# Performance work log

Measured on AMD Instinct MI355X. Metric: run time of the kernel, lower is better.

The kernel has to match this reference:

```python
import jax, jax.numpy as jnp
import numpy as np

NUM_CLASSES = 3
EPS = 1e-6
POS_IOU = 0.5   # assumed thresholds of utils.match_anchors_to_targets
NEG_IOU = 0.4
NEG_RATIO = 3


def _make_anchors(H, W, stride):
    sizes = np.array([3.0, 4.0, 5.0]) * stride  # 3 anchors per location
    ys = (np.arange(H) + 0.5) * stride
    xs = (np.arange(W) + 0.5) * stride
    cy, cx = np.meshgrid(ys, xs, indexing='ij')
    cx = cx[:, :, None]
    cy = cy[:, :, None]
    s = sizes[None, None, :]
    boxes = np.stack([cx - s / 2, cy - s / 2, cx + s / 2, cy + s / 2], axis=-1)  # [H,W,A,4]
    return boxes.reshape(-1, 4).astype(np.float32)


def setup_inputs() -> dict:
    key = jax.random.key(0)
    B, G, A, C = 64, 32, 3, NUM_CLASSES
    scales = [(128, 128, 8), (64, 64, 16), (32, 32, 32)]
    ks = jax.random.split(key, 6)
    inp = {}
    for i, (H, W, s) in enumerate(scales):
        inp[f'pred{i}'] = jax.random.normal(ks[i], (B, A * (5 + C), H, W), jnp.float32)
        inp[f'anchors{i}'] = jnp.asarray(_make_anchors(H, W, s))
    c = jax.random.uniform(ks[3], (B, G, 2), minval=100.0, maxval=900.0)
    wh = jax.random.uniform(ks[4], (B, G, 2), minval=16.0, maxval=200.0)
    inp['gt_boxes'] = jnp.concatenate([c - wh / 2, c + wh / 2], axis=-1)
    inp['gt_labels'] = jax.random.randint(ks[5], (B, G), 0, C)
    return inp


def _smooth_l1(x):
    ax = jnp.abs(x)
    return jnp.where(ax < 1.0, 0.5 * x * x, ax - 0.5)


def _bce_logits(x, t):
    return jnp.maximum(x, 0.0) - x * t + jnp.log1p(jnp.exp(-jnp.abs(x)))


def _pairwise_iou(a, b):  # a [N,4], b [G,4] -> [N,G]
    lt = jnp.maximum(a[:, None, :2], b[None, :, :2])
    rb = jnp.minimum(a[:, None, 2:], b[None, :, 2:])
    wh = jnp.clip(rb - lt, 0.0)
    inter = wh[..., 0] * wh[..., 1]
    area_a = (a[:, 2] - a[:, 0]) * (a[:, 3] - a[:, 1])
    area_b = (b[:, 2] - b[:, 0]) * (b[:, 3] - b[:, 1])
    return inter / (area_a[:, None] + area_b[None, :] - inter + 1e-9)


def _per_image(p, anc, gtb, gtl):
    # p: [N, 5+C], anc: [N,4], gtb: [G,4], gtl: [G]
    iou = _pairwise_iou(anc, gtb)
    best_iou = jnp.max(iou, axis=1)
    best_idx = jnp.argmax(iou, axis=1)
    m_boxes = gtb[best_idx]
    m_labels = gtl[best_idx]
    pos = best_iou >= POS_IOU
    neg = best_iou < NEG_IOU
    posf = pos.astype(p.dtype)

    ax = (anc[:, 0] + anc[:, 2]) * 0.5
    ay = (anc[:, 1] + anc[:, 3]) * 0.5
    aw = jnp.maximum(anc[:, 2] - anc[:, 0], EPS)
    ah = jnp.maximum(anc[:, 3] - anc[:, 1], EPS)
    gx = (m_boxes[:, 0] + m_boxes[:, 2]) * 0.5
    gy = (m_boxes[:, 1] + m_boxes[:, 3]) * 0.5
    gw = jnp.maximum(m_boxes[:, 2] - m_boxes[:, 0], EPS)
    gh = jnp.maximum(m_boxes[:, 3] - m_boxes[:, 1], EPS)
    t_tx = (gx - ax) / aw
    t_ty = (gy - ay) / ah
    t_tw = jnp.log(gw / aw)
    t_th = jnp.log(gh / ah)

    loc = (posf * (_smooth_l1(p[:, 0] - t_tx) + _smooth_l1(p[:, 1] - t_ty)
                   + _smooth_l1(p[:, 2] - t_tw) + _smooth_l1(p[:, 3] - t_th))).sum()

    obj_all = _bce_logits(p[:, 4], posf)
    # hard negative mining on detached loss: top (3*max(1,num_pos)) negatives
    num_pos = pos.sum()
    num_keep = NEG_RATIO * jnp.maximum(1, num_pos)
    neg_loss = jnp.where(neg, jax.lax.stop_gradient(obj_all), -1e9)
    order = jnp.argsort(-neg_loss)
    N = order.shape[0]
    ranks = jnp.zeros((N,), dtype=jnp.int32).at[order].set(jnp.arange(N, dtype=jnp.int32))
    selected = neg & (ranks < num_keep)
    obj = (obj_all * (posf + selected.astype(p.dtype))).sum()

    logp = jax.nn.log_softmax(p[:, 5:], axis=-1)
    tgt = jnp.maximum(m_labels, 0)
    ce = -jnp.take_along_axis(logp, tgt[:, None], axis=1)[:, 0]
    cls = (posf * ce).sum()
    return loc, obj, cls


def reference(pred0, pred1, pred2, anchors0, anchors1, anchors2, gt_boxes, gt_labels):
    B = pred0.shape[0]
    C = NUM_CLASSES
    total = jnp.float32(0.0)
    for pred, anc in ((pred0, anchors0), (pred1, anchors1), (pred2, anchors2)):
        N = anc.shape[0]
        p = pred.transpose(0, 2, 3, 1).reshape(B, N, 5 + C)  # [B, H*W*A, 5+C]
        loc, obj, cls = jax.vmap(lambda pb, gb, gl, a=anc: _per_image(pb, a, gb, gl))(
            p, gt_boxes, gt_labels)
        total = total + loc.sum() + obj.sum() + cls.sum()
    return total / jnp.maximum(1.0, float(B))
```

## Files before the change

kernel.cpp:

```cpp
#include <hip/hip_runtime.h>
#include <math.h>

#define BLK 256
#define SBLK 1024
#define NBINS 2048
#define CSH 42
#define QMASK ((1ULL << CSH) - 1ULL)

__device__ __forceinline__ float bce_logits(float x, float t){
    return fmaxf(x, 0.f) - x * t + log1pf(expf(-fabsf(x)));
}
__device__ __forceinline__ float smooth_l1(float x){
    float ax = fabsf(x);
    return ax < 1.f ? 0.5f * x * x : ax - 0.5f;
}

__global__ __launch_bounds__(BLK)
void det_map_all(const float* __restrict__ pred0,
                 const float* __restrict__ pred1,
                 const float* __restrict__ pred2,
                 const float* __restrict__ gtb,
                 const int*   __restrict__ gtl,
                 float* __restrict__ vals,
                 int*   __restrict__ pos_cnt,
                 double* __restrict__ accum,
                 int B)
{
    const int b  = blockIdx.y;
    const int bx = blockIdx.x;

    const float* pred; int s, qloc, P, logW; float stride_f; size_t vbase;
    if (bx < 48){      s=0; pred=pred0; P=16384; logW=7; stride_f= 8.f; qloc= bx      << 8; vbase=(size_t)b*49152; }
    else if (bx < 60){ s=1; pred=pred1; P= 4096; logW=6; stride_f=16.f; qloc=(bx-48) << 8; vbase=(size_t)B*49152 + (size_t)b*12288; }
    else {             s=2; pred=pred2; P= 1024; logW=5; stride_f=32.f; qloc=(bx-60) << 8; vbase=(size_t)B*49152 + (size_t)B*12288 + (size_t)b*3072; }

    const int tid = threadIdx.x;
    const int lq  = 2*logW - 2;
    const int Q4  = 1 << lq;
    const int a   = qloc >> lq;
    const int q   = qloc - a*Q4 + tid;
    const int pix0 = q << 2;

    const float half = 0.5f * (float)(3 + a) * stride_f;

    const int pixLo = (qloc - a*Q4) << 2;
    const int y0 = pixLo >> logW, y1 = (pixLo + BLK*4 - 1) >> logW;
    const float ymin = ((float)y0 + 0.5f) * stride_f - half;
    const float ymax = ((float)y1 + 0.5f) * stride_f + half;

    __shared__ float4 sg[32];
    __shared__ float  sarea[32];
    __shared__ int    sl[32];
    __shared__ int    s_cnt;

    {
        bool keep = false; float4 G;
        if (tid < 32){
            G = ((const float4*)gtb)[b * 32 + tid];
            keep = (G.y < ymax) && (G.w > ymin);
        }
        unsigned long long m = __ballot(keep);
        if (tid < 64){
            if (keep){
                int idx = (int)__popcll(m & ((1ULL << tid) - 1ULL));
                sg[idx] = G;
                sarea[idx] = (G.z - G.x) * (G.w - G.y);
                sl[idx] = gtl[b * 32 + tid];
            }
            if (tid == 0) s_cnt = (int)__popcll(m);
        }
    }
    __syncthreads();
    const int cnt = s_cnt;

    const int x0 = pix0 & ((1 << logW) - 1);
    const int y  = pix0 >> logW;
    const float cy = ((float)y + 0.5f) * stride_f;
    const float Ay = cy - half, Aw2 = cy + half;
    const float sz = 2.f * half;
    const float area_a = sz * sz;

    float ax[4], az[4];
    #pragma unroll
    for (int j = 0; j < 4; ++j){
        float cx = ((float)(x0 + j) + 0.5f) * stride_f;
        ax[j] = cx - half; az[j] = cx + half;
    }

    float bi[4] = {-1.f, -1.f, -1.f, -1.f};
    float bd[4] = { 1.f,  1.f,  1.f,  1.f};
    int   bg[4] = {0, 0, 0, 0};

    for (int g = 0; g < cnt; ++g){
        const float4 G = sg[g];
        const float sab = area_a + sarea[g];
        const float lty = fmaxf(Ay, G.y);
        const float rby = fminf(Aw2, G.w);
        const float h = fmaxf(rby - lty, 0.f);
        #pragma unroll
        for (int j = 0; j < 4; ++j){
            float ltx = fmaxf(ax[j], G.x);
            float rbx = fminf(az[j], G.z);
            float w = fmaxf(rbx - ltx, 0.f);
            float inter = w * h;
            float d = (sab - inter) + 1e-9f;
            if (inter * bd[j] > bi[j] * d){ bi[j] = inter; bd[j] = d; bg[j] = g; }
        }
    }

    const size_t cP = (size_t)P;
    const float* pp = pred + ((size_t)b * 24 + (size_t)a * 8) * cP + (size_t)pix0;
    const float4 p4v = *(const float4*)(pp + 4 * cP);
    const float p4a[4] = {p4v.x, p4v.y, p4v.z, p4v.w};

    float vout[4];
    float loss = 0.f; int pc = 0;
    #pragma unroll
    for (int j = 0; j < 4; ++j){
        const bool pos = 2.f * bi[j] >= bd[j];
        const bool neg = bi[j] < 0.4f * bd[j];
        vout[j] = neg ? bce_logits(p4a[j], 0.f) : -1.f;
        if (pos){
            pc++;
            const float4 G = sg[bg[j]];
            float axc = (ax[j] + az[j]) * 0.5f, ayc = (Ay + Aw2) * 0.5f;
            float aw = fmaxf(az[j] - ax[j], 1e-6f), ah = fmaxf(Aw2 - Ay, 1e-6f);
            float gxc = (G.x + G.z) * 0.5f, gyc = (G.y + G.w) * 0.5f;
            float gw = fmaxf(G.z - G.x, 1e-6f), gh = fmaxf(G.w - G.y, 1e-6f);
            float p0 = pp[0 * cP + j];
            float p1 = pp[1 * cP + j];
            float p2 = pp[2 * cP + j];
            float p3 = pp[3 * cP + j];
            loss += smooth_l1(p0 - (gxc - axc) / aw);
            loss += smooth_l1(p1 - (gyc - ayc) / ah);
            loss += smooth_l1(p2 - logf(gw / aw));
            loss += smooth_l1(p3 - logf(gh / ah));
            loss += bce_logits(p4a[j], 1.f);
            float c0 = pp[5 * cP + j];
            float c1 = pp[6 * cP + j];
            float c2 = pp[7 * cP + j];
            float m = fmaxf(c0, fmaxf(c1, c2));
            float lse = m + logf(expf(c0 - m) + expf(c1 - m) + expf(c2 - m));
            int tg = sl[bg[j]];
            float ct = (tg == 0) ? c0 : ((tg == 1) ? c1 : c2);
            loss += lse - ct;
        }
    }
    float4 vo = {vout[0], vout[1], vout[2], vout[3]};
    *(float4*)(vals + vbase + ((size_t)(qloc + tid)) * 4) = vo;

    for (int off = 32; off > 0; off >>= 1){
        loss += __shfl_down(loss, off);
        pc   += __shfl_down(pc, off);
    }
    __shared__ float wsum[BLK / 64];
    __shared__ int   wcnt[BLK / 64];
    if ((tid & 63) == 0){ wsum[tid >> 6] = loss; wcnt[tid >> 6] = pc; }
    __syncthreads();
    if (tid == 0){
        float S = 0.f; int C = 0;
        for (int i = 0; i < BLK / 64; ++i){ S += wsum[i]; C += wcnt[i]; }
        if (S != 0.f) atomicAdd(accum, (double)S);
        if (C) atomicAdd(&pos_cnt[s * B + b], C);
    }
}

__global__ __launch_bounds__(SBLK)
void det_select(const float* __restrict__ vals,
                const int* __restrict__ pos_cnt,
                double* __restrict__ accum,
                int B)
{
    const int sb = blockIdx.x;
    const int s = sb / B, b = sb - s * B;
    const int N = (s == 0) ? 49152 : (s == 1) ? 12288 : 3072;
    size_t base = 0;
    if (s >= 1) base += (size_t)B * 49152;
    if (s >= 2) base += (size_t)B * 12288;
    const float* V = vals + base + (size_t)b * (size_t)N;

    const int tid = threadIdx.x;
    const int lane = tid & 63, w = tid >> 6;
    const int rep = w & 1;

    __shared__ unsigned long long h[2][NBINS];
    __shared__ unsigned long long waveT[16];
    __shared__ unsigned long long waveOff[17];
    __shared__ unsigned long long sh_aboveQ;
    __shared__ int sh_b1, sh_rem, sh_done;

    if (tid == 0){
        sh_rem = 3 * max(1, pos_cnt[sb]);
        sh_done = 0; sh_aboveQ = 0ULL; sh_b1 = 0;
    }

    for (int round = 0; round < 2; ++round){
        for (int i = tid; i < NBINS; i += SBLK){ h[0][i] = 0ULL; h[1][i] = 0ULL; }
        __syncthreads();
        const int b1 = sh_b1;

        for (int i = tid * 4; i < N; i += SBLK * 4){
            float4 v4 = *(const float4*)(V + i);
            #pragma unroll
            for (int j = 0; j < 4; ++j){
                float v = (j == 0) ? v4.x : (j == 1) ? v4.y : (j == 2) ? v4.z : v4.w;
                if (!(v >= 0.f)) continue;
                float t = v * 256.f;
                int bin0 = min((int)t, NBINS - 1);
                int key;
                if (round == 0) key = bin0;
                else {
                    if (bin0 != b1) continue;
                    float frac = t - (float)bin0;
                    key = min((int)(frac * 2048.f), NBINS - 1);
                }
                unsigned long long p = (1ULL << CSH) |
                    (unsigned long long)(unsigned)(int)(v * 4194304.f);
                atomicAdd(&h[rep][key], p);
            }
        }
        __syncthreads();

        const int bhi = NBINS - 1 - 2 * tid;
        const unsigned long long c0p = h[0][bhi] + h[1][bhi];
        const unsigned long long c1p = h[0][bhi - 1] + h[1][bhi - 1];
        const unsigned long long pair = c0p + c1p;
        unsigned long long ci = pair;
        #pragma unroll
        for (int off = 1; off < 64; off <<= 1){
            unsigned long long cu = __shfl_up(ci, off);
            if (lane >= off) ci += cu;
        }
        if (lane == 63) waveT[w] = ci;
        __syncthreads();
        if (tid == 0){
            unsigned long long acc = 0ULL;
            #pragma unroll
            for (int i = 0; i < 16; ++i){ waveOff[i] = acc; acc += waveT[i]; }
            waveOff[16] = acc;
            if (round == 0 && sh_rem >= (int)(acc >> CSH)){
                sh_done = 1;
                atomicAdd(accum, (double)(acc & QMASK) * (1.0 / 4194304.0));
            }
        }
        __syncthreads();
        if (sh_done) return;

        const int rem = sh_rem;
        const unsigned long long giP = waveOff[w] + ci;
        const unsigned long long geP = giP - pair;
        const int gi = (int)(giP >> CSH);
        const int ge = (int)(geP >> CSH);
        if (ge < rem && rem <= gi){
            const int c0 = (int)(c0p >> CSH);
            int bin, aboveC; unsigned long long aboveQ;
            if (ge + c0 >= rem){ bin = bhi;     aboveC = ge;      aboveQ = geP & QMASK; }
            else               { bin = bhi - 1; aboveC = ge + c0; aboveQ = (geP + c0p) & QMASK; }
            const int newRem = rem - aboveC;
            if (round == 0){
                sh_b1 = bin; sh_rem = newRem; sh_aboveQ = aboveQ;
            } else {
                float thresh = (float)sh_b1 * (1.f / 256.f) + (float)bin * (1.f / 524288.f);
                double total = (double)(sh_aboveQ + aboveQ) * (1.0 / 4194304.0)
                             + (double)newRem * (double)thresh;
                atomicAdd(accum, total);
            }
        }
        __syncthreads();
    }
}

__global__ void det_finalize(const double* __restrict__ accum,
                             float* __restrict__ out, float inv_b)
{
    if (threadIdx.x == 0) out[0] = (float)(accum[0] * (double)inv_b);
}

extern "C" void kernel_launch(void* const* d_in, const int* in_sizes, int n_in,
                              void* d_out, int out_size, void* d_ws, size_t ws_size,
                              hipStream_t stream)
{
    const float* gtb = (const float*)d_in[6];
    const int*   gtl = (const int*)d_in[7];
    const int B = in_sizes[6] / (32 * 4);

    double* accum = (double*)d_ws;
    int*    pcnt  = (int*)((char*)d_ws + 16);
    float*  vals  = (float*)((char*)d_ws + 1024);

    hipMemsetAsync(d_ws, 0, 1024, stream);

    det_map_all<<<dim3(63, B), BLK, 0, stream>>>(
        (const float*)d_in[0], (const float*)d_in[2], (const float*)d_in[4],
        gtb, gtl, vals, pcnt, accum, B);
    det_select<<<dim3(3 * B), SBLK, 0, stream>>>(vals, pcnt, accum, B);
    det_finalize<<<dim3(1), 64, 0, stream>>>(accum, (float*)d_out, 1.0f / (float)B);
}
```

Measured before the change: 210.2 us.

## Fuse anchor matching and hard-negative selection into one per-image kernel

```diff
diff --git a/kernel.cpp b/kernel.cpp
--- a/kernel.cpp
+++ b/kernel.cpp
@@ -1,9 +1,9 @@
 #include <hip/hip_runtime.h>
 #include <math.h>
 
-#define BLK 256
-#define SBLK 1024
+#define FBLK 1024
 #define NBINS 2048
+#define NREP 4
 #define CSH 42
 #define QMASK ((1ULL << CSH) - 1ULL)
 
@@ -15,215 +15,206 @@
     return ax < 1.f ? 0.5f * x * x : ax - 0.5f;
 }
 
-__global__ __launch_bounds__(BLK)
-void det_map_all(const float* __restrict__ pred0,
-                 const float* __restrict__ pred1,
-                 const float* __restrict__ pred2,
-                 const float* __restrict__ gtb,
-                 const int*   __restrict__ gtl,
-                 float* __restrict__ vals,
-                 int*   __restrict__ pos_cnt,
-                 double* __restrict__ accum,
-                 int B)
+struct SharedBlk {
+    float4 sg[16][32];
+    float  sarea[16][32];
+    int    sl[16][32];
+    unsigned long long hist[NREP][NBINS];
+    unsigned long long waveT[16];
+    unsigned long long waveOff[17];
+    float  wsum[16];
+    int    wcnt[16];
+    double sh_sel;
+    float  sh_map;
+    int    sh_K, sh_b1, sh_rem, sh_done;
+    unsigned long long sh_aboveQ;
+};
+
+template<int NIT, int ACT>
+__device__ __forceinline__ void map_phase(
+    const float* __restrict__ pred, int b, int P, int logW, float stride_f,
+    const float4* __restrict__ sgw, const float* __restrict__ sareaw,
+    const int* __restrict__ slw, int cnt, int w, int lane,
+    float4* v, float& loss, int& pc)
 {
-    const int b  = blockIdx.y;
-    const int bx = blockIdx.x;
-
-    const float* pred; int s, qloc, P, logW; float stride_f; size_t vbase;
-    if (bx < 48){      s=0; pred=pred0; P=16384; logW=7; stride_f= 8.f; qloc= bx      << 8; vbase=(size_t)b*49152; }
-    else if (bx < 60){ s=1; pred=pred1; P= 4096; logW=6; stride_f=16.f; qloc=(bx-48) << 8; vbase=(size_t)B*49152 + (size_t)b*12288; }
-    else {             s=2; pred=pred2; P= 1024; logW=5; stride_f=32.f; qloc=(bx-60) << 8; vbase=(size_t)B*49152 + (size_t)B*12288 + (size_t)b*3072; }
-
-    const int tid = threadIdx.x;
-    const int lq  = 2*logW - 2;
-    const int Q4  = 1 << lq;
-    const int a   = qloc >> lq;
-    const int q   = qloc - a*Q4 + tid;
-    const int pix0 = q << 2;
-
-    const float half = 0.5f * (float)(3 + a) * stride_f;
-
-    const int pixLo = (qloc - a*Q4) << 2;
-    const int y0 = pixLo >> logW, y1 = (pixLo + BLK*4 - 1) >> logW;
-    const float ymin = ((float)y0 + 0.5f) * stride_f - half;
-    const float ymax = ((float)y1 + 0.5f) * stride_f + half;
-
-    __shared__ float4 sg[32];
-    __shared__ float  sarea[32];
-    __shared__ int    sl[32];
-    __shared__ int    s_cnt;
-
+    const int Qp16 = (P >> 2) >> 4;
+    loss = 0.f; pc = 0;
+    #pragma unroll
+    for (int a = 0; a < 3; ++a){
+        const float half = 0.5f * (float)(3 + a) * stride_f;
+        const float sz = 2.f * half;
+        const float area_a = sz * sz;
+        #pragma unroll
+        for (int it = 0; it < NIT; ++it){
+            float4 res = make_float4(-1.f, -1.f, -1.f, -1.f);
+            if (ACT == 64 || lane < ACT){
+                const int quad = w * Qp16 + it * 64 + lane;
+                const int pix0 = quad << 2;
+                const int x0 = pix0 & ((1 << logW) - 1);
+                const int y  = pix0 >> logW;
+                const float cy = ((float)y + 0.5f) * stride_f;
+                const float Ay = cy - half, Ay2 = cy + half;
+                float ax[4], az[4];
+                #pragma unroll
+                for (int j = 0; j < 4; ++j){
+                    float cx = ((float)(x0 + j) + 0.5f) * stride_f;
+                    ax[j] = cx - half; az[j] = cx + half;
+                }
+                float bi[4] = {-1.f,-1.f,-1.f,-1.f};
+                float bd[4] = { 1.f, 1.f, 1.f, 1.f};
+                int   bg[4] = {0,0,0,0};
+                for (int g = 0; g < cnt; ++g){
+                    const float4 G = sgw[g];
+                    const float sab = area_a + sareaw[g];
+                    const float h = fmaxf(fminf(Ay2, G.w) - fmaxf(Ay, G.y), 0.f);
+                    #pragma unroll
+                    for (int j = 0; j < 4; ++j){
+                        float wdt = fmaxf(fminf(az[j], G.z) - fmaxf(ax[j], G.x), 0.f);
+                        float inter = wdt * h;
+                        float d = (sab - inter) + 1e-9f;
+                        if (inter * bd[j] > bi[j] * d){ bi[j] = inter; bd[j] = d; bg[j] = g; }
+                    }
+                }
+                const size_t cP = (size_t)P;
+                const float* pp = pred + ((size_t)b * 24 + (size_t)a * 8) * cP + (size_t)pix0;
+                const float4 p4v = *(const float4*)(pp + 4 * cP);
+                const float p4a[4] = {p4v.x, p4v.y, p4v.z, p4v.w};
+                float vout[4];
+                #pragma unroll
+                for (int j = 0; j < 4; ++j){
+                    const bool pos = 2.f * bi[j] >= bd[j];
+                    const bool neg = bi[j] < 0.4f * bd[j];
+                    vout[j] = neg ? bce_logits(p4a[j], 0.f) : -1.f;
+                    if (pos){
+                        pc++;
+                        const float4 G = sgw[bg[j]];
+                        float axc = (ax[j] + az[j]) * 0.5f, ayc = (Ay + Ay2) * 0.5f;
+                        float aw = fmaxf(az[j] - ax[j], 1e-6f), ah = fmaxf(Ay2 - Ay, 1e-6f);
+                        float gxc = (G.x + G.z) * 0.5f, gyc = (G.y + G.w) * 0.5f;
+                        float gw = fmaxf(G.z - G.x, 1e-6f), gh = fmaxf(G.w - G.y, 1e-6f);
+                        float p0 = pp[0 * cP + j];
+                        float p1 = pp[1 * cP + j];
+                        float p2 = pp[2 * cP + j];
+                        float p3 = pp[3 * cP + j];
+                        loss += smooth_l1(p0 - (gxc - axc) / aw);
+                        loss += smooth_l1(p1 - (gyc - ayc) / ah);
+                        loss += smooth_l1(p2 - logf(gw / aw));
+                        loss += smooth_l1(p3 - logf(gh / ah));
+                        loss += bce_logits(p4a[j], 1.f);
+                        float c0 = pp[5 * cP + j];
+                        float c1 = pp[6 * cP + j];
+                        float c2 = pp[7 * cP + j];
+                        float m = fmaxf(c0, fmaxf(c1, c2));
+                        float lse = m + logf(expf(c0 - m) + expf(c1 - m) + expf(c2 - m));
+                        int tg = slw[bg[j]];
+                        float ct = (tg == 0) ? c0 : ((tg == 1) ? c1 : c2);
+                        loss += lse - ct;
+                    }
+                }
+                res = make_float4(vout[0], vout[1], vout[2], vout[3]);
+            }
+            v[a * NIT + it] = res;
+        }
+    }
+}
+
+__device__ __forceinline__ void bin_val(float vv, int round, int b1,
+                                        unsigned long long* histrep)
+{
+    if (!(vv >= 0.f)) return;
+    float t = vv * 256.f;
+    int bin0 = min((int)t, NBINS - 1);
+    int key;
+    if (round == 0) key = bin0;
+    else {
+        if (bin0 != b1) return;
+        float frac = t - (float)bin0;
+        key = min((int)(frac * 2048.f), NBINS - 1);
+    }
+    unsigned long long p = (1ULL << CSH) |
+        (unsigned long long)(unsigned)(int)(vv * 4194304.f);
+    atomicAdd(&histrep[key], p);
+}
+
+__global__ __launch_bounds__(FBLK, 4)
+void det_fused(const float* __restrict__ p0, const float* __restrict__ p1,
+               const float* __restrict__ p2,
+               const float* __restrict__ gtb, const int* __restrict__ gtl,
+               double* __restrict__ accum, unsigned* __restrict__ done_cnt,
+               float* __restrict__ out, int B)
+{
+    __shared__ SharedBlk S;
+    const int sb = blockIdx.x;
+    const int s = sb / B, b = sb - s * B;
+    const int tid = threadIdx.x, lane = tid & 63, w = tid >> 6;
+
+    const float* pred = (s == 0) ? p0 : (s == 1) ? p1 : p2;
+    const int P       = (s == 0) ? 16384 : (s == 1) ? 4096 : 1024;
+    const int logW    = (s == 0) ? 7 : (s == 1) ? 6 : 5;
+    const float stf   = (s == 0) ? 8.f : (s == 1) ? 16.f : 32.f;
+
+    const int H = P >> logW;
+    const int rpw = H >> 4;
+    const float half_max = 2.5f * stf;
+    const float ymin = ((float)(w * rpw) + 0.5f) * stf - half_max;
+    const float ymax = ((float)(w * rpw + rpw - 1) + 0.5f) * stf + half_max;
+    int cnt;
     {
         bool keep = false; float4 G;
-        if (tid < 32){
-            G = ((const float4*)gtb)[b * 32 + tid];
+        if (lane < 32){
+            G = ((const float4*)gtb)[b * 32 + lane];
             keep = (G.y < ymax) && (G.w > ymin);
         }
         unsigned long long m = __ballot(keep);
-        if (tid < 64){
-            if (keep){
-                int idx = (int)__popcll(m & ((1ULL << tid) - 1ULL));
-                sg[idx] = G;
-                sarea[idx] = (G.z - G.x) * (G.w - G.y);
-                sl[idx] = gtl[b * 32 + tid];
-            }
-            if (tid == 0) s_cnt = (int)__popcll(m);
-        }
-    }
-    __syncthreads();
-    const int cnt = s_cnt;
-
-    const int x0 = pix0 & ((1 << logW) - 1);
-    const int y  = pix0 >> logW;
-    const float cy = ((float)y + 0.5f) * stride_f;
-    const float Ay = cy - half, Aw2 = cy + half;
-    const float sz = 2.f * half;
-    const float area_a = sz * sz;
-
-    float ax[4], az[4];
+        if (keep){
+            int idx = (int)__popcll(m & ((1ULL << lane) - 1ULL));
+            S.sg[w][idx] = G;
+            S.sarea[w][idx] = (G.z - G.x) * (G.w - G.y);
+            S.sl[w][idx] = gtl[b * 32 + lane];
+        }
+        cnt = (int)__popcll(m);
+    }
+
+    float4 v[12];
     #pragma unroll
-    for (int j = 0; j < 4; ++j){
-        float cx = ((float)(x0 + j) + 0.5f) * stride_f;
-        ax[j] = cx - half; az[j] = cx + half;
-    }
-
-    float bi[4] = {-1.f, -1.f, -1.f, -1.f};
-    float bd[4] = { 1.f,  1.f,  1.f,  1.f};
-    int   bg[4] = {0, 0, 0, 0};
-
-    for (int g = 0; g < cnt; ++g){
-        const float4 G = sg[g];
-        const float sab = area_a + sarea[g];
-        const float lty = fmaxf(Ay, G.y);
-        const float rby = fminf(Aw2, G.w);
-        const float h = fmaxf(rby - lty, 0.f);
-        #pragma unroll
-        for (int j = 0; j < 4; ++j){
-            float ltx = fmaxf(ax[j], G.x);
-            float rbx = fminf(az[j], G.z);
-            float w = fmaxf(rbx - ltx, 0.f);
-            float inter = w * h;
-            float d = (sab - inter) + 1e-9f;
-            if (inter * bd[j] > bi[j] * d){ bi[j] = inter; bd[j] = d; bg[j] = g; }
-        }
-    }
-
-    const size_t cP = (size_t)P;
-    const float* pp = pred + ((size_t)b * 24 + (size_t)a * 8) * cP + (size_t)pix0;
-    const float4 p4v = *(const float4*)(pp + 4 * cP);
-    const float p4a[4] = {p4v.x, p4v.y, p4v.z, p4v.w};
-
-    float vout[4];
-    float loss = 0.f; int pc = 0;
-    #pragma unroll
-    for (int j = 0; j < 4; ++j){
-        const bool pos = 2.f * bi[j] >= bd[j];
-        const bool neg = bi[j] < 0.4f * bd[j];
-        vout[j] = neg ? bce_logits(p4a[j], 0.f) : -1.f;
-        if (pos){
-            pc++;
-            const float4 G = sg[bg[j]];
-            float axc = (ax[j] + az[j]) * 0.5f, ayc = (Ay + Aw2) * 0.5f;
-            float aw = fmaxf(az[j] - ax[j], 1e-6f), ah = fmaxf(Aw2 - Ay, 1e-6f);
-            float gxc = (G.x + G.z) * 0.5f, gyc = (G.y + G.w) * 0.5f;
-            float gw = fmaxf(G.z - G.x, 1e-6f), gh = fmaxf(G.w - G.y, 1e-6f);
-            float p0 = pp[0 * cP + j];
-            float p1 = pp[1 * cP + j];
-            float p2 = pp[2 * cP + j];
-            float p3 = pp[3 * cP + j];
-            loss += smooth_l1(p0 - (gxc - axc) / aw);
-            loss += smooth_l1(p1 - (gyc - ayc) / ah);
-            loss += smooth_l1(p2 - logf(gw / aw));
-            loss += smooth_l1(p3 - logf(gh / ah));
-            loss += bce_logits(p4a[j], 1.f);
-            float c0 = pp[5 * cP + j];
-            float c1 = pp[6 * cP + j];
-            float c2 = pp[7 * cP + j];
-            float m = fmaxf(c0, fmaxf(c1, c2));
-            float lse = m + logf(expf(c0 - m) + expf(c1 - m) + expf(c2 - m));
-            int tg = sl[bg[j]];
-            float ct = (tg == 0) ? c0 : ((tg == 1) ? c1 : c2);
-            loss += lse - ct;
-        }
-    }
-    float4 vo = {vout[0], vout[1], vout[2], vout[3]};
-    *(float4*)(vals + vbase + ((size_t)(qloc + tid)) * 4) = vo;
-
+    for (int k = 0; k < 12; ++k) v[k] = make_float4(-1.f,-1.f,-1.f,-1.f);
+    float mloss; int pc;
+    if (s == 0)      map_phase<4,64>(pred,b,P,logW,stf,S.sg[w],S.sarea[w],S.sl[w],cnt,w,lane,v,mloss,pc);
+    else if (s == 1) map_phase<1,64>(pred,b,P,logW,stf,S.sg[w],S.sarea[w],S.sl[w],cnt,w,lane,v,mloss,pc);
+    else             map_phase<1,16>(pred,b,P,logW,stf,S.sg[w],S.sarea[w],S.sl[w],cnt,w,lane,v,mloss,pc);
+
+    for (int i = tid; i < NREP * NBINS; i += FBLK)
+        ((unsigned long long*)S.hist)[i] = 0ULL;
     for (int off = 32; off > 0; off >>= 1){
-        loss += __shfl_down(loss, off);
-        pc   += __shfl_down(pc, off);
-    }
-    __shared__ float wsum[BLK / 64];
-    __shared__ int   wcnt[BLK / 64];
-    if ((tid & 63) == 0){ wsum[tid >> 6] = loss; wcnt[tid >> 6] = pc; }
+        mloss += __shfl_down(mloss, off);
+        pc    += __shfl_down(pc, off);
+    }
+    if (lane == 0){ S.wsum[w] = mloss; S.wcnt[w] = pc; }
     __syncthreads();
     if (tid == 0){
-        float S = 0.f; int C = 0;
-        for (int i = 0; i < BLK / 64; ++i){ S += wsum[i]; C += wcnt[i]; }
-        if (S != 0.f) atomicAdd(accum, (double)S);
-        if (C) atomicAdd(&pos_cnt[s * B + b], C);
-    }
-}
-
-__global__ __launch_bounds__(SBLK)
-void det_select(const float* __restrict__ vals,
-                const int* __restrict__ pos_cnt,
-                double* __restrict__ accum,
-                int B)
-{
-    const int sb = blockIdx.x;
-    const int s = sb / B, b = sb - s * B;
-    const int N = (s == 0) ? 49152 : (s == 1) ? 12288 : 3072;
-    size_t base = 0;
-    if (s >= 1) base += (size_t)B * 49152;
-    if (s >= 2) base += (size_t)B * 12288;
-    const float* V = vals + base + (size_t)b * (size_t)N;
-
-    const int tid = threadIdx.x;
-    const int lane = tid & 63, w = tid >> 6;
-    const int rep = w & 1;
-
-    __shared__ unsigned long long h[2][NBINS];
-    __shared__ unsigned long long waveT[16];
-    __shared__ unsigned long long waveOff[17];
-    __shared__ unsigned long long sh_aboveQ;
-    __shared__ int sh_b1, sh_rem, sh_done;
-
-    if (tid == 0){
-        sh_rem = 3 * max(1, pos_cnt[sb]);
-        sh_done = 0; sh_aboveQ = 0ULL; sh_b1 = 0;
-    }
-
-    for (int round = 0; round < 2; ++round){
-        for (int i = tid; i < NBINS; i += SBLK){ h[0][i] = 0ULL; h[1][i] = 0ULL; }
-        __syncthreads();
-        const int b1 = sh_b1;
-
-        for (int i = tid * 4; i < N; i += SBLK * 4){
-            float4 v4 = *(const float4*)(V + i);
-            #pragma unroll
-            for (int j = 0; j < 4; ++j){
-                float v = (j == 0) ? v4.x : (j == 1) ? v4.y : (j == 2) ? v4.z : v4.w;
-                if (!(v >= 0.f)) continue;
-                float t = v * 256.f;
-                int bin0 = min((int)t, NBINS - 1);
-                int key;
-                if (round == 0) key = bin0;
-                else {
-                    if (bin0 != b1) continue;
-                    float frac = t - (float)bin0;
-                    key = min((int)(frac * 2048.f), NBINS - 1);
-                }
-                unsigned long long p = (1ULL << CSH) |
-                    (unsigned long long)(unsigned)(int)(v * 4194304.f);
-                atomicAdd(&h[rep][key], p);
-            }
-        }
-        __syncthreads();
-
-        const int bhi = NBINS - 1 - 2 * tid;
-        const unsigned long long c0p = h[0][bhi] + h[1][bhi];
-        const unsigned long long c1p = h[0][bhi - 1] + h[1][bhi - 1];
+        float Ls = 0.f; int C = 0;
+        for (int i = 0; i < 16; ++i){ Ls += S.wsum[i]; C += S.wcnt[i]; }
+        S.sh_map = Ls; S.sh_K = 3 * max(1, C);
+        S.sh_done = 0; S.sh_sel = 0.0;
+    }
+    __syncthreads();
+
+    unsigned long long* histrep = S.hist[w & (NREP - 1)];
+
+    #pragma unroll
+    for (int k = 0; k < 12; ++k){
+        bin_val(v[k].x, 0, 0, histrep);
+        bin_val(v[k].y, 0, 0, histrep);
+        bin_val(v[k].z, 0, 0, histrep);
+        bin_val(v[k].w, 0, 0, histrep);
+    }
+    __syncthreads();
+
+    const int bhi = NBINS - 1 - 2 * tid;
+    {
+        unsigned long long c0p = 0ULL, c1p = 0ULL;
+        #pragma unroll
+        for (int r = 0; r < NREP; ++r){ c0p += S.hist[r][bhi]; c1p += S.hist[r][bhi - 1]; }
         const unsigned long long pair = c0p + c1p;
         unsigned long long ci = pair;
         #pragma unroll
@@ -231,23 +222,71 @@
             unsigned long long cu = __shfl_up(ci, off);
             if (lane >= off) ci += cu;
         }
-        if (lane == 63) waveT[w] = ci;
+        if (lane == 63) S.waveT[w] = ci;
         __syncthreads();
         if (tid == 0){
             unsigned long long acc = 0ULL;
             #pragma unroll
-            for (int i = 0; i < 16; ++i){ waveOff[i] = acc; acc += waveT[i]; }
-            waveOff[16] = acc;
-            if (round == 0 && sh_rem >= (int)(acc >> CSH)){
-                sh_done = 1;
-                atomicAdd(accum, (double)(acc & QMASK) * (1.0 / 4194304.0));
+            for (int i = 0; i < 16; ++i){ S.waveOff[i] = acc; acc += S.waveT[i]; }
+            S.waveOff[16] = acc;
+            if (S.sh_K >= (int)(acc >> CSH)){
+                S.sh_done = 1;
+                S.sh_sel = (double)(acc & QMASK) * (1.0 / 4194304.0);
             }
         }
         __syncthreads();
-        if (sh_done) return;
-
-        const int rem = sh_rem;
-        const unsigned long long giP = waveOff[w] + ci;
+        if (!S.sh_done){
+            const int rem = S.sh_K;
+            const unsigned long long giP = S.waveOff[w] + ci;
+            const unsigned long long geP = giP - pair;
+            const int gi = (int)(giP >> CSH);
+            const int ge = (int)(geP >> CSH);
+            if (ge < rem && rem <= gi){
+                const int c0 = (int)(c0p >> CSH);
+                int bin, aboveC; unsigned long long aboveQ;
+                if (ge + c0 >= rem){ bin = bhi;     aboveC = ge;      aboveQ = geP & QMASK; }
+                else               { bin = bhi - 1; aboveC = ge + c0; aboveQ = (geP + c0p) & QMASK; }
+                S.sh_b1 = bin; S.sh_rem = rem - aboveC; S.sh_aboveQ = aboveQ;
+            }
+        }
+    }
+    __syncthreads();
+
+    if (!S.sh_done){
+        for (int i = tid; i < NREP * NBINS; i += FBLK)
+            ((unsigned long long*)S.hist)[i] = 0ULL;
+        __syncthreads();
+        const int b1 = S.sh_b1;
+        #pragma unroll
+        for (int k = 0; k < 12; ++k){
+            bin_val(v[k].x, 1, b1, histrep);
+            bin_val(v[k].y, 1, b1, histrep);
+            bin_val(v[k].z, 1, b1, histrep);
+            bin_val(v[k].w, 1, b1, histrep);
+        }
+        __syncthreads();
+
+        unsigned long long c0p = 0ULL, c1p = 0ULL;
+        #pragma unroll
+        for (int r = 0; r < NREP; ++r){ c0p += S.hist[r][bhi]; c1p += S.hist[r][bhi - 1]; }
+        const unsigned long long pair = c0p + c1p;
+        unsigned long long ci = pair;
+        #pragma unroll
+        for (int off = 1; off < 64; off <<= 1){
+            unsigned long long cu = __shfl_up(ci, off);
+            if (lane >= off) ci += cu;
+        }
+        if (lane == 63) S.waveT[w] = ci;
+        __syncthreads();
+        if (tid == 0){
+            unsigned long long acc = 0ULL;
+            #pragma unroll
+            for (int i = 0; i < 16; ++i){ S.waveOff[i] = acc; acc += S.waveT[i]; }
+            S.waveOff[16] = acc;
+        }
+        __syncthreads();
+        const int rem = S.sh_rem;
+        const unsigned long long giP = S.waveOff[w] + ci;
         const unsigned long long geP = giP - pair;
         const int gi = (int)(giP >> CSH);
         const int ge = (int)(geP >> CSH);
@@ -257,23 +296,23 @@
             if (ge + c0 >= rem){ bin = bhi;     aboveC = ge;      aboveQ = geP & QMASK; }
             else               { bin = bhi - 1; aboveC = ge + c0; aboveQ = (geP + c0p) & QMASK; }
             const int newRem = rem - aboveC;
-            if (round == 0){
-                sh_b1 = bin; sh_rem = newRem; sh_aboveQ = aboveQ;
-            } else {
-                float thresh = (float)sh_b1 * (1.f / 256.f) + (float)bin * (1.f / 524288.f);
-                double total = (double)(sh_aboveQ + aboveQ) * (1.0 / 4194304.0)
-                             + (double)newRem * (double)thresh;
-                atomicAdd(accum, total);
-            }
-        }
-        __syncthreads();
-    }
-}
-
-__global__ void det_finalize(const double* __restrict__ accum,
-                             float* __restrict__ out, float inv_b)
-{
-    if (threadIdx.x == 0) out[0] = (float)(accum[0] * (double)inv_b);
+            float thresh = (float)S.sh_b1 * (1.f / 256.f) + (float)bin * (1.f / 524288.f);
+            S.sh_sel = (double)(S.sh_aboveQ + aboveQ) * (1.0 / 4194304.0)
+                     + (double)newRem * (double)thresh;
+        }
+        __syncthreads();
+    }
+
+    if (tid == 0){
+        atomicAdd(accum, (double)S.sh_map + S.sh_sel);
+        __threadfence();
+        unsigned t = atomicAdd(done_cnt, 1u);
+        if (t == (unsigned)(3 * B - 1)){
+            __threadfence();
+            double tot = atomicAdd(accum, 0.0);
+            out[0] = (float)(tot / (double)B);
+        }
+    }
 }
 
 extern "C" void kernel_launch(void* const* d_in, const int* in_sizes, int n_in,
@@ -284,15 +323,12 @@
     const int*   gtl = (const int*)d_in[7];
     const int B = in_sizes[6] / (32 * 4);
 
-    double* accum = (double*)d_ws;
-    int*    pcnt  = (int*)((char*)d_ws + 16);
-    float*  vals  = (float*)((char*)d_ws + 1024);
-
-    hipMemsetAsync(d_ws, 0, 1024, stream);
-
-    det_map_all<<<dim3(63, B), BLK, 0, stream>>>(
+    double*   accum = (double*)d_ws;
+    unsigned* done  = (unsigned*)((char*)d_ws + 8);
+
+    hipMemsetAsync(d_ws, 0, 16, stream);
+
+    det_fused<<<dim3(3 * B), FBLK, 0, stream>>>(
         (const float*)d_in[0], (const float*)d_in[2], (const float*)d_in[4],
-        gtb, gtl, vals, pcnt, accum, B);
-    det_select<<<dim3(3 * B), SBLK, 0, stream>>>(vals, pcnt, accum, B);
-    det_finalize<<<dim3(1), 64, 0, stream>>>(accum, (float*)d_out, 1.0f / (float)B);
-}
+        gtb, gtl, accum, done, (float*)d_out, B);
+}
```

After: 265.6 us. 26.4% more time.

## Build negative-loss histograms in map kernel and fold finalize into single-pass select

Applied to the files above, without the earlier changes.

```diff
diff --git a/kernel.cpp b/kernel.cpp
--- a/kernel.cpp
+++ b/kernel.cpp
@@ -3,7 +3,8 @@
 
 #define BLK 256
 #define SBLK 1024
-#define NBINS 2048
+#define HBINS 16384
+#define BPT 16
 #define CSH 42
 #define QMASK ((1ULL << CSH) - 1ULL)
 
@@ -21,7 +22,7 @@
                  const float* __restrict__ pred2,
                  const float* __restrict__ gtb,
                  const int*   __restrict__ gtl,
-                 float* __restrict__ vals,
+                 unsigned long long* __restrict__ hist,
                  int*   __restrict__ pos_cnt,
                  double* __restrict__ accum,
                  int B)
@@ -29,10 +30,10 @@
     const int b  = blockIdx.y;
     const int bx = blockIdx.x;
 
-    const float* pred; int s, qloc, P, logW; float stride_f; size_t vbase;
-    if (bx < 48){      s=0; pred=pred0; P=16384; logW=7; stride_f= 8.f; qloc= bx      << 8; vbase=(size_t)b*49152; }
-    else if (bx < 60){ s=1; pred=pred1; P= 4096; logW=6; stride_f=16.f; qloc=(bx-48) << 8; vbase=(size_t)B*49152 + (size_t)b*12288; }
-    else {             s=2; pred=pred2; P= 1024; logW=5; stride_f=32.f; qloc=(bx-60) << 8; vbase=(size_t)B*49152 + (size_t)B*12288 + (size_t)b*3072; }
+    const float* pred; int s, qloc, P, logW; float stride_f;
+    if (bx < 48){      s=0; pred=pred0; P=16384; logW=7; stride_f= 8.f; qloc= bx      << 8; }
+    else if (bx < 60){ s=1; pred=pred1; P= 4096; logW=6; stride_f=16.f; qloc=(bx-48) << 8; }
+    else {             s=2; pred=pred2; P= 1024; logW=5; stride_f=32.f; qloc=(bx-60) << 8; }
 
     const int tid = threadIdx.x;
     const int lq  = 2*logW - 2;
@@ -76,7 +77,7 @@
     const int x0 = pix0 & ((1 << logW) - 1);
     const int y  = pix0 >> logW;
     const float cy = ((float)y + 0.5f) * stride_f;
-    const float Ay = cy - half, Aw2 = cy + half;
+    const float Ay = cy - half, Ay2 = cy + half;
     const float sz = 2.f * half;
     const float area_a = sz * sz;
 
@@ -94,15 +95,11 @@
     for (int g = 0; g < cnt; ++g){
         const float4 G = sg[g];
         const float sab = area_a + sarea[g];
-        const float lty = fmaxf(Ay, G.y);
-        const float rby = fminf(Aw2, G.w);
-        const float h = fmaxf(rby - lty, 0.f);
+        const float h = fmaxf(fminf(Ay2, G.w) - fmaxf(Ay, G.y), 0.f);
         #pragma unroll
         for (int j = 0; j < 4; ++j){
-            float ltx = fmaxf(ax[j], G.x);
-            float rbx = fminf(az[j], G.z);
-            float w = fmaxf(rbx - ltx, 0.f);
-            float inter = w * h;
+            float wdt = fmaxf(fminf(az[j], G.z) - fmaxf(ax[j], G.x), 0.f);
+            float inter = wdt * h;
             float d = (sab - inter) + 1e-9f;
             if (inter * bd[j] > bi[j] * d){ bi[j] = inter; bd[j] = d; bg[j] = g; }
         }
@@ -113,18 +110,25 @@
     const float4 p4v = *(const float4*)(pp + 4 * cP);
     const float p4a[4] = {p4v.x, p4v.y, p4v.z, p4v.w};
 
-    float vout[4];
+    unsigned long long* H = hist + (size_t)(s * B + b) * HBINS;
+
     float loss = 0.f; int pc = 0;
     #pragma unroll
     for (int j = 0; j < 4; ++j){
         const bool pos = 2.f * bi[j] >= bd[j];
         const bool neg = bi[j] < 0.4f * bd[j];
-        vout[j] = neg ? bce_logits(p4a[j], 0.f) : -1.f;
+        if (neg){
+            float v = bce_logits(p4a[j], 0.f);
+            int bin = min((int)(v * 2048.f), HBINS - 1);
+            unsigned long long p = (1ULL << CSH) |
+                (unsigned long long)(unsigned)(int)(v * 4194304.f);
+            atomicAdd(&H[bin], p);
+        }
         if (pos){
             pc++;
             const float4 G = sg[bg[j]];
-            float axc = (ax[j] + az[j]) * 0.5f, ayc = (Ay + Aw2) * 0.5f;
-            float aw = fmaxf(az[j] - ax[j], 1e-6f), ah = fmaxf(Aw2 - Ay, 1e-6f);
+            float axc = (ax[j] + az[j]) * 0.5f, ayc = (Ay + Ay2) * 0.5f;
+            float aw = fmaxf(az[j] - ax[j], 1e-6f), ah = fmaxf(Ay2 - Ay, 1e-6f);
             float gxc = (G.x + G.z) * 0.5f, gyc = (G.y + G.w) * 0.5f;
             float gw = fmaxf(G.z - G.x, 1e-6f), gh = fmaxf(G.w - G.y, 1e-6f);
             float p0 = pp[0 * cP + j];
@@ -146,8 +150,6 @@
             loss += lse - ct;
         }
     }
-    float4 vo = {vout[0], vout[1], vout[2], vout[3]};
-    *(float4*)(vals + vbase + ((size_t)(qloc + tid)) * 4) = vo;
 
     for (int off = 32; off > 0; off >>= 1){
         loss += __shfl_down(loss, off);
@@ -166,114 +168,83 @@
 }
 
 __global__ __launch_bounds__(SBLK)
-void det_select(const float* __restrict__ vals,
-                const int* __restrict__ pos_cnt,
-                double* __restrict__ accum,
-                int B)
+void det_select_hist(const unsigned long long* __restrict__ hist,
+                     const int* __restrict__ pos_cnt,
+                     double* __restrict__ accum,
+                     unsigned* __restrict__ done_cnt,
+                     float* __restrict__ out, int B)
 {
     const int sb = blockIdx.x;
-    const int s = sb / B, b = sb - s * B;
-    const int N = (s == 0) ? 49152 : (s == 1) ? 12288 : 3072;
-    size_t base = 0;
-    if (s >= 1) base += (size_t)B * 49152;
-    if (s >= 2) base += (size_t)B * 12288;
-    const float* V = vals + base + (size_t)b * (size_t)N;
-
-    const int tid = threadIdx.x;
-    const int lane = tid & 63, w = tid >> 6;
-    const int rep = w & 1;
-
-    __shared__ unsigned long long h[2][NBINS];
+    const unsigned long long* H = hist + (size_t)sb * HBINS;
+    const int tid = threadIdx.x, lane = tid & 63, w = tid >> 6;
+
+    const int K = 3 * max(1, pos_cnt[sb]);
+
+    const int start = HBINS - BPT * (tid + 1);
+    unsigned long long chunk[BPT];
+    unsigned long long tot = 0ULL;
+    #pragma unroll
+    for (int i = 0; i < BPT; ++i){ chunk[i] = H[start + i]; tot += chunk[i]; }
+
+    const unsigned long long chunkP = tot;
+    unsigned long long ci = tot;
+    #pragma unroll
+    for (int off = 1; off < 64; off <<= 1){
+        unsigned long long cu = __shfl_up(ci, off);
+        if (lane >= off) ci += cu;
+    }
     __shared__ unsigned long long waveT[16];
     __shared__ unsigned long long waveOff[17];
-    __shared__ unsigned long long sh_aboveQ;
-    __shared__ int sh_b1, sh_rem, sh_done;
-
+    __shared__ double sh_sel;
+    __shared__ int sh_done;
+    if (lane == 63) waveT[w] = ci;
+    if (tid == 0) sh_done = 0;
+    __syncthreads();
     if (tid == 0){
-        sh_rem = 3 * max(1, pos_cnt[sb]);
-        sh_done = 0; sh_aboveQ = 0ULL; sh_b1 = 0;
-    }
-
-    for (int round = 0; round < 2; ++round){
-        for (int i = tid; i < NBINS; i += SBLK){ h[0][i] = 0ULL; h[1][i] = 0ULL; }
-        __syncthreads();
-        const int b1 = sh_b1;
-
-        for (int i = tid * 4; i < N; i += SBLK * 4){
-            float4 v4 = *(const float4*)(V + i);
-            #pragma unroll
-            for (int j = 0; j < 4; ++j){
-                float v = (j == 0) ? v4.x : (j == 1) ? v4.y : (j == 2) ? v4.z : v4.w;
-                if (!(v >= 0.f)) continue;
-                float t = v * 256.f;
-                int bin0 = min((int)t, NBINS - 1);
-                int key;
-                if (round == 0) key = bin0;
-                else {
-                    if (bin0 != b1) continue;
-                    float frac = t - (float)bin0;
-                    key = min((int)(frac * 2048.f), NBINS - 1);
-                }
-                unsigned long long p = (1ULL << CSH) |
-                    (unsigned long long)(unsigned)(int)(v * 4194304.f);
-                atomicAdd(&h[rep][key], p);
-            }
-        }
-        __syncthreads();
-
-        const int bhi = NBINS - 1 - 2 * tid;
-        const unsigned long long c0p = h[0][bhi] + h[1][bhi];
-        const unsigned long long c1p = h[0][bhi - 1] + h[1][bhi - 1];
-        const unsigned long long pair = c0p + c1p;
-        unsigned long long ci = pair;
+        unsigned long long acc = 0ULL;
         #pragma unroll
-        for (int off = 1; off < 64; off <<= 1){
-            unsigned long long cu = __shfl_up(ci, off);
-            if (lane >= off) ci += cu;
-        }
-        if (lane == 63) waveT[w] = ci;
-        __syncthreads();
-        if (tid == 0){
-            unsigned long long acc = 0ULL;
-            #pragma unroll
-            for (int i = 0; i < 16; ++i){ waveOff[i] = acc; acc += waveT[i]; }
-            waveOff[16] = acc;
-            if (round == 0 && sh_rem >= (int)(acc >> CSH)){
-                sh_done = 1;
-                atomicAdd(accum, (double)(acc & QMASK) * (1.0 / 4194304.0));
-            }
-        }
-        __syncthreads();
-        if (sh_done) return;
-
-        const int rem = sh_rem;
+        for (int i = 0; i < 16; ++i){ waveOff[i] = acc; acc += waveT[i]; }
+        waveOff[16] = acc;
+        if (K >= (int)(acc >> CSH)){
+            sh_done = 1;
+            sh_sel = (double)(acc & QMASK) * (1.0 / 4194304.0);
+        }
+    }
+    __syncthreads();
+
+    if (!sh_done){
         const unsigned long long giP = waveOff[w] + ci;
-        const unsigned long long geP = giP - pair;
+        const unsigned long long geP = giP - chunkP;
         const int gi = (int)(giP >> CSH);
         const int ge = (int)(geP >> CSH);
-        if (ge < rem && rem <= gi){
-            const int c0 = (int)(c0p >> CSH);
-            int bin, aboveC; unsigned long long aboveQ;
-            if (ge + c0 >= rem){ bin = bhi;     aboveC = ge;      aboveQ = geP & QMASK; }
-            else               { bin = bhi - 1; aboveC = ge + c0; aboveQ = (geP + c0p) & QMASK; }
-            const int newRem = rem - aboveC;
-            if (round == 0){
-                sh_b1 = bin; sh_rem = newRem; sh_aboveQ = aboveQ;
-            } else {
-                float thresh = (float)sh_b1 * (1.f / 256.f) + (float)bin * (1.f / 524288.f);
-                double total = (double)(sh_aboveQ + aboveQ) * (1.0 / 4194304.0)
-                             + (double)newRem * (double)thresh;
-                atomicAdd(accum, total);
+        if (ge < K && K <= gi){
+            int aboveC = ge;
+            unsigned long long aboveQ = geP & QMASK;
+            int bin = start; int rem = 0;
+            #pragma unroll
+            for (int i = BPT - 1; i >= 0; --i){
+                int c = (int)(chunk[i] >> CSH);
+                if (aboveC + c >= K){ bin = start + i; rem = K - aboveC; break; }
+                aboveC += c;
+                aboveQ += chunk[i] & QMASK;
             }
+            float thresh = (float)bin * (1.f / 2048.f);
+            sh_sel = (double)aboveQ * (1.0 / 4194304.0)
+                   + (double)rem * (double)thresh;
         }
         __syncthreads();
     }
-}
-
-__global__ void det_finalize(const double* __restrict__ accum,
-                             float* __restrict__ out, float inv_b)
-{
-    if (threadIdx.x == 0) out[0] = (float)(accum[0] * (double)inv_b);
+
+    if (tid == 0){
+        atomicAdd(accum, sh_sel);
+        __threadfence();
+        unsigned t = atomicAdd(done_cnt, 1u);
+        if (t == (unsigned)gridDim.x - 1u){
+            __threadfence();
+            double totd = atomicAdd(accum, 0.0);
+            out[0] = (float)(totd / (double)B);
+        }
+    }
 }
 
 extern "C" void kernel_launch(void* const* d_in, const int* in_sizes, int n_in,
@@ -284,15 +255,16 @@
     const int*   gtl = (const int*)d_in[7];
     const int B = in_sizes[6] / (32 * 4);
 
-    double* accum = (double*)d_ws;
-    int*    pcnt  = (int*)((char*)d_ws + 16);
-    float*  vals  = (float*)((char*)d_ws + 1024);
-
-    hipMemsetAsync(d_ws, 0, 1024, stream);
+    double*   accum = (double*)d_ws;
+    unsigned* done  = (unsigned*)((char*)d_ws + 8);
+    int*      pcnt  = (int*)((char*)d_ws + 16);
+    unsigned long long* hist = (unsigned long long*)((char*)d_ws + 1024);
+
+    hipMemsetAsync(d_ws, 0, 1024 + (size_t)(3 * B) * HBINS * 8, stream);
 
     det_map_all<<<dim3(63, B), BLK, 0, stream>>>(
         (const float*)d_in[0], (const float*)d_in[2], (const float*)d_in[4],
-        gtb, gtl, vals, pcnt, accum, B);
-    det_select<<<dim3(3 * B), SBLK, 0, stream>>>(vals, pcnt, accum, B);
-    det_finalize<<<dim3(1), 64, 0, stream>>>(accum, (float*)d_out, 1.0f / (float)B);
-}
+        gtb, gtl, hist, pcnt, accum, B);
+    det_select_hist<<<dim3(3 * B), SBLK, 0, stream>>>(
+        hist, pcnt, accum, done, (float*)d_out, B);
+}
```

Result: slower. 348.8 us (+65.9%).

## Replace global atomics and finalize kernel with per-block slots and last-block reduction

Applied to the files above, without the earlier changes.

```diff
diff --git a/kernel.cpp b/kernel.cpp
--- a/kernel.cpp
+++ b/kernel.cpp
@@ -22,8 +22,9 @@
                  const float* __restrict__ gtb,
                  const int*   __restrict__ gtl,
                  float* __restrict__ vals,
-                 int*   __restrict__ pos_cnt,
-                 double* __restrict__ accum,
+                 float* __restrict__ loss_slot,
+                 int*   __restrict__ pcnt_slot,
+                 unsigned* __restrict__ done_cnt,
                  int B)
 {
     const int b  = blockIdx.y;
@@ -76,7 +77,7 @@
     const int x0 = pix0 & ((1 << logW) - 1);
     const int y  = pix0 >> logW;
     const float cy = ((float)y + 0.5f) * stride_f;
-    const float Ay = cy - half, Aw2 = cy + half;
+    const float Ay = cy - half, Ay2 = cy + half;
     const float sz = 2.f * half;
     const float area_a = sz * sz;
 
@@ -94,15 +95,11 @@
     for (int g = 0; g < cnt; ++g){
         const float4 G = sg[g];
         const float sab = area_a + sarea[g];
-        const float lty = fmaxf(Ay, G.y);
-        const float rby = fminf(Aw2, G.w);
-        const float h = fmaxf(rby - lty, 0.f);
+        const float h = fmaxf(fminf(Ay2, G.w) - fmaxf(Ay, G.y), 0.f);
         #pragma unroll
         for (int j = 0; j < 4; ++j){
-            float ltx = fmaxf(ax[j], G.x);
-            float rbx = fminf(az[j], G.z);
-            float w = fmaxf(rbx - ltx, 0.f);
-            float inter = w * h;
+            float wdt = fmaxf(fminf(az[j], G.z) - fmaxf(ax[j], G.x), 0.f);
+            float inter = wdt * h;
             float d = (sab - inter) + 1e-9f;
             if (inter * bd[j] > bi[j] * d){ bi[j] = inter; bd[j] = d; bg[j] = g; }
         }
@@ -123,8 +120,8 @@
         if (pos){
             pc++;
             const float4 G = sg[bg[j]];
-            float axc = (ax[j] + az[j]) * 0.5f, ayc = (Ay + Aw2) * 0.5f;
-            float aw = fmaxf(az[j] - ax[j], 1e-6f), ah = fmaxf(Aw2 - Ay, 1e-6f);
+            float axc = (ax[j] + az[j]) * 0.5f, ayc = (Ay + Ay2) * 0.5f;
+            float aw = fmaxf(az[j] - ax[j], 1e-6f), ah = fmaxf(Ay2 - Ay, 1e-6f);
             float gxc = (G.x + G.z) * 0.5f, gyc = (G.y + G.w) * 0.5f;
             float gw = fmaxf(G.z - G.x, 1e-6f), gh = fmaxf(G.w - G.y, 1e-6f);
             float p0 = pp[0 * cP + j];
@@ -147,7 +144,7 @@
         }
     }
     float4 vo = {vout[0], vout[1], vout[2], vout[3]};
-    *(float4*)(vals + vbase + ((size_t)(qloc + tid)) * 4) = vo;
+    *(float4*)(vals + vbase + ((size_t)(qloc - a*Q4 + tid + a*Q4)) * 4) = vo;
 
     for (int off = 32; off > 0; off >>= 1){
         loss += __shfl_down(loss, off);
@@ -160,16 +157,19 @@
     if (tid == 0){
         float S = 0.f; int C = 0;
         for (int i = 0; i < BLK / 64; ++i){ S += wsum[i]; C += wcnt[i]; }
-        if (S != 0.f) atomicAdd(accum, (double)S);
-        if (C) atomicAdd(&pos_cnt[s * B + b], C);
+        loss_slot[b * 63 + bx] = S;
+        pcnt_slot[b * 63 + bx] = C;
+        if (b == 0 && bx == 0) *done_cnt = 0u;
     }
 }
 
 __global__ __launch_bounds__(SBLK)
 void det_select(const float* __restrict__ vals,
-                const int* __restrict__ pos_cnt,
-                double* __restrict__ accum,
-                int B)
+                const float* __restrict__ loss_slot,
+                const int* __restrict__ pcnt_slot,
+                double* __restrict__ slice_tot,
+                unsigned* __restrict__ done_cnt,
+                float* __restrict__ out, int B)
 {
     const int sb = blockIdx.x;
     const int s = sb / B, b = sb - s * B;
@@ -187,11 +187,25 @@
     __shared__ unsigned long long waveT[16];
     __shared__ unsigned long long waveOff[17];
     __shared__ unsigned long long sh_aboveQ;
-    __shared__ int sh_b1, sh_rem, sh_done;
-
-    if (tid == 0){
-        sh_rem = 3 * max(1, pos_cnt[sb]);
-        sh_done = 0; sh_aboveQ = 0ULL; sh_b1 = 0;
+    __shared__ double sh_sel;
+    __shared__ float sh_ml;
+    __shared__ int sh_b1, sh_rem, sh_done, sh_K, sh_last;
+
+    {
+        const int nb   = (s == 0) ? 48 : (s == 1) ? 12 : 3;
+        const int off0 = b * 63 + ((s == 0) ? 0 : (s == 1) ? 48 : 60);
+        float ml = 0.f; int C = 0;
+        if (tid < nb){ ml = loss_slot[off0 + tid]; C = pcnt_slot[off0 + tid]; }
+        if (tid < 64){
+            for (int off = 32; off > 0; off >>= 1){
+                ml += __shfl_down(ml, off);
+                C  += __shfl_down(C, off);
+            }
+            if (tid == 0){
+                sh_ml = ml; sh_K = 3 * max(1, C);
+                sh_rem = sh_K; sh_done = 0;
+            }
+        }
     }
 
     for (int round = 0; round < 2; ++round){
@@ -199,27 +213,30 @@
         __syncthreads();
         const int b1 = sh_b1;
 
-        for (int i = tid * 4; i < N; i += SBLK * 4){
-            float4 v4 = *(const float4*)(V + i);
-            #pragma unroll
-            for (int j = 0; j < 4; ++j){
-                float v = (j == 0) ? v4.x : (j == 1) ? v4.y : (j == 2) ? v4.z : v4.w;
-                if (!(v >= 0.f)) continue;
-                float t = v * 256.f;
-                int bin0 = min((int)t, NBINS - 1);
-                int key;
-                if (round == 0) key = bin0;
-                else {
-                    if (bin0 != b1) continue;
-                    float frac = t - (float)bin0;
-                    key = min((int)(frac * 2048.f), NBINS - 1);
+        if (round == 0 || !sh_done){
+            for (int i = tid * 4; i < N; i += SBLK * 4){
+                float4 v4 = *(const float4*)(V + i);
+                #pragma unroll
+                for (int j = 0; j < 4; ++j){
+                    float v = (j == 0) ? v4.x : (j == 1) ? v4.y : (j == 2) ? v4.z : v4.w;
+                    if (!(v >= 0.f)) continue;
+                    float t = v * 256.f;
+                    int bin0 = min((int)t, NBINS - 1);
+                    int key;
+                    if (round == 0) key = bin0;
+                    else {
+                        if (bin0 != b1) continue;
+                        float frac = t - (float)bin0;
+                        key = min((int)(frac * 2048.f), NBINS - 1);
+                    }
+                    unsigned long long p = (1ULL << CSH) |
+                        (unsigned long long)(unsigned)(int)(v * 4194304.f);
+                    atomicAdd(&h[rep][key], p);
                 }
-                unsigned long long p = (1ULL << CSH) |
-                    (unsigned long long)(unsigned)(int)(v * 4194304.f);
-                atomicAdd(&h[rep][key], p);
-            }
-        }
-        __syncthreads();
+            }
+        }
+        __syncthreads();
+        if (sh_done) break;
 
         const int bhi = NBINS - 1 - 2 * tid;
         const unsigned long long c0p = h[0][bhi] + h[1][bhi];
@@ -238,13 +255,13 @@
             #pragma unroll
             for (int i = 0; i < 16; ++i){ waveOff[i] = acc; acc += waveT[i]; }
             waveOff[16] = acc;
-            if (round == 0 && sh_rem >= (int)(acc >> CSH)){
+            if (round == 0 && sh_K >= (int)(acc >> CSH)){
                 sh_done = 1;
-                atomicAdd(accum, (double)(acc & QMASK) * (1.0 / 4194304.0));
-            }
-        }
-        __syncthreads();
-        if (sh_done) return;
+                sh_sel = (double)(acc & QMASK) * (1.0 / 4194304.0);
+            }
+        }
+        __syncthreads();
+        if (sh_done) break;
 
         const int rem = sh_rem;
         const unsigned long long giP = waveOff[w] + ci;
@@ -261,19 +278,33 @@
                 sh_b1 = bin; sh_rem = newRem; sh_aboveQ = aboveQ;
             } else {
                 float thresh = (float)sh_b1 * (1.f / 256.f) + (float)bin * (1.f / 524288.f);
-                double total = (double)(sh_aboveQ + aboveQ) * (1.0 / 4194304.0)
-                             + (double)newRem * (double)thresh;
-                atomicAdd(accum, total);
-            }
-        }
-        __syncthreads();
-    }
-}
-
-__global__ void det_finalize(const double* __restrict__ accum,
-                             float* __restrict__ out, float inv_b)
-{
-    if (threadIdx.x == 0) out[0] = (float)(accum[0] * (double)inv_b);
+                sh_sel = (double)(sh_aboveQ + aboveQ) * (1.0 / 4194304.0)
+                       + (double)newRem * (double)thresh;
+            }
+        }
+        __syncthreads();
+    }
+
+    if (tid == 0){
+        slice_tot[sb] = (double)sh_ml + sh_sel;
+        __threadfence();
+        unsigned t = atomicAdd(done_cnt, 1u);
+        sh_last = (t == (unsigned)(gridDim.x - 1));
+        if (sh_last) __threadfence();
+    }
+    __syncthreads();
+    if (sh_last){
+        double p = (tid < 3 * B) ? slice_tot[tid] : 0.0;
+        for (int off = 32; off > 0; off >>= 1) p += __shfl_down(p, off);
+        __shared__ double wred[16];
+        if (lane == 0) wred[w] = p;
+        __syncthreads();
+        if (tid == 0){
+            double tot = 0.0;
+            for (int i = 0; i < 16; ++i) tot += wred[i];
+            out[0] = (float)(tot / (double)B);
+        }
+    }
 }
 
 extern "C" void kernel_launch(void* const* d_in, const int* in_sizes, int n_in,
@@ -284,15 +315,15 @@
     const int*   gtl = (const int*)d_in[7];
     const int B = in_sizes[6] / (32 * 4);
 
-    double* accum = (double*)d_ws;
-    int*    pcnt  = (int*)((char*)d_ws + 16);
-    float*  vals  = (float*)((char*)d_ws + 1024);
-
-    hipMemsetAsync(d_ws, 0, 1024, stream);
+    unsigned* done      = (unsigned*)d_ws;
+    double*   slice_tot = (double*)((char*)d_ws + 64);
+    float*    loss_slot = (float*)((char*)d_ws + 2048);
+    int*      pcnt_slot = (int*)((char*)d_ws + 2048 + 16384);
+    float*    vals      = (float*)((char*)d_ws + 36864);
 
     det_map_all<<<dim3(63, B), BLK, 0, stream>>>(
         (const float*)d_in[0], (const float*)d_in[2], (const float*)d_in[4],
-        gtb, gtl, vals, pcnt, accum, B);
-    det_select<<<dim3(3 * B), SBLK, 0, stream>>>(vals, pcnt, accum, B);
-    det_finalize<<<dim3(1), 64, 0, stream>>>(accum, (float*)d_out, 1.0f / (float)B);
-}
+        gtb, gtl, vals, loss_slot, pcnt_slot, done, B);
+    det_select<<<dim3(3 * B), SBLK, 0, stream>>>(
+        vals, loss_slot, pcnt_slot, slice_tot, done, (float*)d_out, B);
+}
```

Result: no change. 208.9 us (-0.6%).
